# Performance work log

Hardware: AMD Instinct MI355X
Metric: run time of the kernel (lower is better)

The kernel has to match this reference:

```python
import jax, jax.numpy as jnp
import numpy as np

HID, NQ, NKV, HD = 4096, 32, 8, 128
EPS = 1e-6
GOLDEN = 1.618033988749895
BASE = 10000.0


def _rmsnorm(x, w, eps=EPS):
    var = jnp.mean(x.astype(jnp.float32) ** 2, axis=-1, keepdims=True)
    return (x * jax.lax.rsqrt(var + eps)).astype(x.dtype) * w


def _rope_half(t, pos, inv_freq):
    # t: (B,T,H,dh); pos: (B,T); inv_freq: (dh//2,)
    ang = pos.astype(jnp.float32)[..., None] * inv_freq  # (B,T,dq)
    cos = jnp.cos(ang)[:, :, None, :]
    sin = jnp.sin(ang)[:, :, None, :]
    dq = inv_freq.shape[0]
    t1, t2 = t[..., :dq], t[..., dq:]
    return jnp.concatenate([t1 * cos - t2 * sin, t1 * sin + t2 * cos], axis=-1)


def _apply_ggrope(q, k, row_ids, col_ids):
    # 2D RoPE: first half of head_dim encodes rows, second half encodes cols;
    # column frequencies scaled by the golden ratio (GGRoPE).
    dh = HD // 2
    inv_freq = 1.0 / (BASE ** (jnp.arange(0, dh, 2, dtype=jnp.float32) / dh))
    inv_freq_col = inv_freq * GOLDEN

    def rot(t):
        tr = _rope_half(t[..., :dh], row_ids, inv_freq)
        tc = _rope_half(t[..., dh:], col_ids, inv_freq_col)
        return jnp.concatenate([tr, tc], axis=-1)

    return rot(q), rot(k)


def setup_inputs() -> dict:
    key = jax.random.key(0)
    ks = jax.random.split(key, 9)
    B, T = 1, 2048
    s = 0.02
    return {
        "x": jax.random.normal(ks[0], (B, T, HID), jnp.float32),
        "row_ids": jax.random.randint(ks[1], (B, T), 0, 30),
        "col_ids": jax.random.randint(ks[2], (B, T), 0, 30),
        "attention_mask": jnp.zeros((B, 1, T, T), jnp.float32),
        "Wq": jax.random.normal(ks[3], (HID, NQ * HD), jnp.float32) * s,
        "Wk": jax.random.normal(ks[4], (HID, NKV * HD), jnp.float32) * s,
        "Wv": jax.random.normal(ks[5], (HID, NKV * HD), jnp.float32) * s,
        "Wo": jax.random.normal(ks[6], (NQ * HD, HID), jnp.float32) * s,
        "q_norm_w": jnp.ones((HD,), jnp.float32),
        "k_norm_w": jnp.ones((HD,), jnp.float32),
    }


def reference(x, row_ids, col_ids, attention_mask, Wq, Wk, Wv, Wo, q_norm_w, k_norm_w):
    B, T, _ = x.shape
    group = NQ // NKV
    q = (x @ Wq).reshape(B, T, NQ, HD)
    k = (x @ Wk).reshape(B, T, NKV, HD)
    v = (x @ Wv).reshape(B, T, NKV, HD)
    q = _rmsnorm(q, q_norm_w)
    k = _rmsnorm(k, k_norm_w)
    q, k = _apply_ggrope(q, k, row_ids, col_ids)
    # expand KV heads to match query heads (GQA)
    k = jnp.repeat(k, group, axis=2)  # (B,T,NQ,HD)
    v = jnp.repeat(v, group, axis=2)
    q = q.transpose(0, 2, 1, 3)  # (B,NQ,T,HD)
    k = k.transpose(0, 2, 1, 3)
    v = v.transpose(0, 2, 1, 3)
    ssmax_scale = (HD ** -0.5) * np.log(max(T, 2)).astype(np.float32)
    scores = jnp.einsum("bhqd,bhkd->bhqk", q, k) * ssmax_scale
    scores = scores + attention_mask
    attn = jax.nn.softmax(scores.astype(jnp.float32), axis=-1).astype(q.dtype)
    out = jnp.einsum("bhqk,bhkd->bhqd", attn, v)
    out = out.transpose(0, 2, 1, 3).reshape(B, T, NQ * HD)
    return out @ Wo
```

## Files before the change

kernel.cpp:

```cpp
#include <hip/hip_runtime.h>
#include <hip/hip_bf16.h>

typedef unsigned short u16;
typedef __attribute__((ext_vector_type(8))) short bf16x8;
typedef __attribute__((ext_vector_type(4))) float f32x4;

#define LOG2E_F 1.4426950408889634f
#define QSCALE (0.08838834764831845f * 7.625595228825695f * 1.4426950408889634f)

__device__ __forceinline__ u16 f2bf(float f) {
  unsigned x = __float_as_uint(f);
  unsigned r = (x + 0x7fffu + ((x >> 16) & 1u)) >> 16;
  return (u16)r;
}
__device__ __forceinline__ float bf2f(u16 u) {
  return __uint_as_float(((unsigned)u) << 16);
}
__device__ __forceinline__ float exp2a(float x) {
  float r;
  asm("v_exp_f32 %0, %1" : "=v"(r) : "v"(x));
  return r;
}
__device__ __forceinline__ unsigned cvtpk(float lo, float hi) {
  unsigned r;
  asm("v_cvt_pk_bf16_f32 %0, %1, %2" : "=v"(r) : "v"(lo), "v"(hi));
  return r;
}

__device__ __forceinline__ void gload_lds16(const void* g, void* l) {
  __builtin_amdgcn_global_load_lds(
      (__attribute__((address_space(1))) void*)(g),
      (__attribute__((address_space(3))) void*)(l), 16, 0, 0);
}

__device__ __forceinline__ f32x4 mfma16(bf16x8 a, bf16x8 b, f32x4 c) {
  return __builtin_amdgcn_mfma_f32_16x16x32_bf16(a, b, c, 0, 0, 0);
}

__global__ __launch_bounds__(256) void prep(const float4* __restrict__ x,
                                            ushort4* __restrict__ xb,
                                            const float4* __restrict__ mask,
                                            int* __restrict__ flag,
                                            const int* __restrict__ row_ids,
                                            const int* __restrict__ col_ids,
                                            float4* __restrict__ trig) {
  int bid = blockIdx.x;
  if (bid < 8192) {
    size_t i = (size_t)bid * 256 + threadIdx.x;
    float4 v = x[i];
    ushort4 o;
    o.x = f2bf(v.x); o.y = f2bf(v.y); o.z = f2bf(v.z); o.w = f2bf(v.w);
    xb[i] = o;
  } else if (bid < 12288) {
    size_t i = (size_t)(bid - 8192) * 256 + threadIdx.x;
    float4 v = mask[i];
    if (v.x != 0.f || v.y != 0.f || v.z != 0.f || v.w != 0.f) atomicOr(flag, 1);
  } else {
    int idx = (bid - 12288) * 256 + threadIdx.x;
    int tok = idx >> 5, i = idx & 31;
    float inv = exp2f(-(float)i * 0.41524101186092030f);
    float ar = (float)row_ids[tok] * inv;
    float ac = (float)col_ids[tok] * inv * 1.618033988749895f;
    float4 o;
    o.x = cosf(ar); o.y = sinf(ar); o.z = cosf(ac); o.w = sinf(ac);
    trig[idx] = o;
  }
}

__global__ __launch_bounds__(256) void tcvt_all(const float* __restrict__ Wq,
                                                const float* __restrict__ Wk,
                                                const float* __restrict__ Wv,
                                                const float* __restrict__ Wo,
                                                u16* __restrict__ wqkvt,
                                                u16* __restrict__ wot) {
  __shared__ float t[64][65];
  int bid = blockIdx.x;
  const float* src;
  u16* dst;
  int N;
  if (bid < 4096)      { src = Wq; dst = wqkvt;                         N = 4096; }
  else if (bid < 5120) { src = Wk; dst = wqkvt + (size_t)4096 * 4096;   N = 1024; bid -= 4096; }
  else if (bid < 6144) { src = Wv; dst = wqkvt + (size_t)5120 * 4096;   N = 1024; bid -= 5120; }
  else                 { src = Wo; dst = wot;                           N = 4096; bid -= 6144; }
  int kt = bid & 63, nt = bid >> 6;
  int k0 = kt * 64, n0 = nt * 64;
  int tid = threadIdx.x;
#pragma unroll
  for (int it = 0; it < 16; ++it) {
    int idx = it * 256 + tid;
    int row = idx >> 6, col = idx & 63;
    t[row][col] = src[(size_t)(k0 + row) * N + n0 + col];
  }
  __syncthreads();
#pragma unroll
  for (int it = 0; it < 8; ++it) {
    int idx = it * 256 + tid;
    int nrow = idx >> 5, kc = idx & 31;
    ushort2 o;
    o.x = f2bf(t[kc * 2][nrow]);
    o.y = f2bf(t[kc * 2 + 1][nrow]);
    *(ushort2*)&dst[(size_t)(n0 + nrow) * 4096 + k0 + kc * 2] = o;
  }
}

__global__ __launch_bounds__(256) void rope_kernel(u16* __restrict__ qk,
                                                   const float4* __restrict__ trig,
                                                   const float* __restrict__ qw,
                                                   const float* __restrict__ kw) {
  const int tok = blockIdx.x;
  const int tid = threadIdx.x;
  const int w = tid >> 6, lane = tid & 63;
  float4 t4 = trig[tok * 32 + (lane & 31)];
  float sgn = (lane < 32) ? -1.0f : 1.0f;

  for (int it = 0; it < 10; ++it) {
    int hh = w + it * 4;
    bool isQ = (hh < 32);
    int colbase = isQ ? hh * 128 : 4096 + (hh - 32) * 128;
    const float* nw = isQ ? qw : kw;
    float scale = isQ ? QSCALE : 1.0f;
    u16* p = qk + (size_t)tok * 5120 + colbase;
    float v1 = bf2f(p[lane]);
    float v2 = bf2f(p[64 + lane]);
    float w1 = nw[lane], w2 = nw[64 + lane];
    float ss = v1 * v1 + v2 * v2;
    ss += __shfl_xor(ss, 1);  ss += __shfl_xor(ss, 2);  ss += __shfl_xor(ss, 4);
    ss += __shfl_xor(ss, 8);  ss += __shfl_xor(ss, 16); ss += __shfl_xor(ss, 32);
    float rinv = rsqrtf(ss * (1.0f / 128.0f) + 1e-6f);
    float n1 = v1 * rinv * w1;
    float n2 = v2 * rinv * w2;
    float p1 = __shfl_xor(n1, 32);
    float p2 = __shfl_xor(n2, 32);
    float r1 = n1 * t4.x + sgn * p1 * t4.y;
    float r2 = n2 * t4.z + sgn * p2 * t4.w;
    p[lane]      = f2bf(r1 * scale);
    p[64 + lane] = f2bf(r2 * scale);
  }
}

template <int MODE>
__global__ __launch_bounds__(512, 2) void gemm256(const u16* __restrict__ A,
                                                  const u16* __restrict__ Bt,
                                                  void* __restrict__ C0,
                                                  u16* __restrict__ Vt, int nnt) {
  extern __shared__ char smem[];
  const int tid = threadIdx.x, lane = tid & 63, w = tid >> 6;
  const int l15 = lane & 15, l4 = lane >> 4;
  const int wr = w >> 2, wc = w & 3;
  constexpr int NF = (MODE == 0) ? 3 : 4;
  constexpr int BNW = (MODE == 0) ? 48 : 64;

  int wgid = (blockIdx.x & 7) * (gridDim.x >> 3) + (blockIdx.x >> 3);
  int kh = 0;
  if (MODE == 1) { kh = wgid >> 7; wgid &= 127; }
  const int mt = wgid / nnt, nt = wgid % nnt;
  const int m0 = mt * 256;
  const int n0 = nt * ((MODE == 0) ? 192 : 256);
  const int tbase = kh * 32;

  const int kswz = (((tid & 7) ^ ((tid >> 3) & 7)) << 4);
  const char* arow = (const char*)A + (size_t)(m0 + (tid >> 3)) * 8192 + kswz;
  const char* brow = (const char*)Bt + (size_t)(n0 + (tid >> 3)) * 8192 + kswz;

  auto stageA = [&](int t, int h) {
#pragma unroll
    for (int rd = 0; rd < 2; ++rd)
      gload_lds16(arow + (size_t)(h * 128 + rd * 64) * 8192 + t * 128,
                  smem + ((t & 1) * 2 + h) * 16384 + rd * 8192 + w * 1024);
  };
  auto stageB0 = [&](int t) {
#pragma unroll
    for (int rd = 0; rd < 3; ++rd)
      gload_lds16(brow + (size_t)(rd * 64) * 8192 + t * 128,
                  smem + 65536 + (t & 1) * 24576 + rd * 8192 + w * 1024);
  };
  auto stageB1 = [&](int t, int h) {
#pragma unroll
    for (int rd = 0; rd < 2; ++rd)
      gload_lds16(brow + (size_t)(h * 128 + rd * 64) * 8192 + t * 128,
                  smem + 65536 + ((t & 1) * 2 + h) * 16384 + rd * 8192 + w * 1024);
  };

  f32x4 acc[8][NF];
#pragma unroll
  for (int i = 0; i < 8; ++i)
#pragma unroll
    for (int j = 0; j < NF; ++j) acc[i][j] = (f32x4){0.f, 0.f, 0.f, 0.f};

  const int aoff0 = ((l4) ^ (l15 & 7)) << 4;
  const int aoff1 = ((4 + l4) ^ (l15 & 7)) << 4;

  stageA(tbase, 0); stageA(tbase, 1);
  if constexpr (MODE == 0) {
    stageB0(tbase); stageB0(tbase + 1);
    asm volatile("s_waitcnt vmcnt(3)" ::: "memory");
  } else {
    stageB1(tbase, 0); stageB1(tbase, 1);
    stageB1(tbase + 1, 0); stageB1(tbase + 1, 1);
    asm volatile("s_waitcnt vmcnt(4)" ::: "memory");
  }
  __builtin_amdgcn_s_barrier();

  auto do_iter = [&](int t0, int last) {
    bf16x8 bfr[NF][2];
#pragma unroll
    for (int p = 0; p < 8; ++p) {
      const int s = p >> 2, qd = p & 3;
      const char* aT = smem + (s * 2 + wr) * 16384 + l15 * 128;
      bf16x8 afr[2][2];
#pragma unroll
      for (int jm = 0; jm < 2; ++jm) {
        afr[jm][0] = *(const bf16x8*)(aT + (2 * qd + jm) * 2048 + aoff0);
        afr[jm][1] = *(const bf16x8*)(aT + (2 * qd + jm) * 2048 + aoff1);
      }
      if (qd == 0) {
        const char* bT;
        if constexpr (MODE == 0)
          bT = smem + 65536 + s * 24576 + (wc * 48 + l15) * 128;
        else
          bT = smem + 65536 + (s * 2 + (wc >> 1)) * 16384 +
               ((wc & 1) * 64 + l15) * 128;
#pragma unroll
        for (int nf = 0; nf < NF; ++nf) {
          bfr[nf][0] = *(const bf16x8*)(bT + nf * 2048 + aoff0);
          bfr[nf][1] = *(const bf16x8*)(bT + nf * 2048 + aoff1);
        }
      }
      if (p == 0) { stageA(t0 + 1, 0); stageA(t0 + 1, 1); }
      if (!last) {
        if constexpr (MODE == 0) {
          if (p == 1) stageB0(t0 + 2);
          if (p == 5) stageB0(t0 + 3);
        } else {
          if (p == 1) stageB1(t0 + 2, 0);
          if (p == 2) stageB1(t0 + 2, 1);
          if (p == 5) stageB1(t0 + 3, 0);
          if (p == 6) stageB1(t0 + 3, 1);
        }
        if (p == 4) { stageA(t0 + 2, 0); stageA(t0 + 2, 1); }
      }
      if (p == 3) {
        if (last) asm volatile("s_waitcnt vmcnt(0)" ::: "memory");
        else if constexpr (MODE == 0)
          asm volatile("s_waitcnt vmcnt(3)" ::: "memory");
        else
          asm volatile("s_waitcnt vmcnt(4)" ::: "memory");
      }
      if (p == 7 && !last) {
        if constexpr (MODE == 0)
          asm volatile("s_waitcnt vmcnt(3)" ::: "memory");
        else
          asm volatile("s_waitcnt vmcnt(4)" ::: "memory");
      }
      __builtin_amdgcn_s_barrier();
      asm volatile("s_waitcnt lgkmcnt(0)" ::: "memory");
      __builtin_amdgcn_sched_barrier(0);
      __builtin_amdgcn_s_setprio(1);
#pragma unroll
      for (int ks = 0; ks < 2; ++ks)
#pragma unroll
        for (int jm = 0; jm < 2; ++jm)
#pragma unroll
          for (int nf = 0; nf < NF; ++nf)
            acc[2 * qd + jm][nf] =
                mfma16(afr[jm][ks], bfr[nf][ks], acc[2 * qd + jm][nf]);
      __builtin_amdgcn_s_setprio(0);
      __builtin_amdgcn_s_barrier();
    }
  };

  constexpr int NIT = (MODE == 0) ? 32 : 16;
  for (int j = 0; j < NIT - 1; ++j) do_iter(tbase + 2 * j, 0);
  do_iter(tbase + 2 * (NIT - 1), 1);

  if (MODE == 0) {
    u16* qkp = (u16*)C0;
#pragma unroll
    for (int mf = 0; mf < 8; ++mf)
#pragma unroll
      for (int nf = 0; nf < NF; ++nf) {
        int ng = n0 + wc * BNW + nf * 16 + l15;
        if (ng < 5120) {
#pragma unroll
          for (int r = 0; r < 4; ++r) {
            int mg = m0 + wr * 128 + mf * 16 + l4 * 4 + r;
            qkp[(size_t)mg * 5120 + ng] = f2bf(acc[mf][nf][r]);
          }
        } else {
          int vr = ng - 5120;
          int mg = m0 + wr * 128 + mf * 16 + l4 * 4;
          ushort4 pk;
          pk.x = f2bf(acc[mf][nf][0]); pk.y = f2bf(acc[mf][nf][1]);
          pk.z = f2bf(acc[mf][nf][2]); pk.w = f2bf(acc[mf][nf][3]);
          *(ushort4*)&Vt[(size_t)vr * 2048 + mg] = pk;
        }
      }
  } else {
    float* Cp = (float*)C0 + (size_t)kh * 8388608;
#pragma unroll
    for (int mf = 0; mf < 8; ++mf)
#pragma unroll
      for (int nf = 0; nf < NF; ++nf) {
        int ng = n0 + wc * BNW + nf * 16 + l15;
#pragma unroll
        for (int r = 0; r < 4; ++r) {
          int mg = m0 + wr * 128 + mf * 16 + l4 * 4 + r;
          Cp[(size_t)mg * 4096 + ng] = acc[mf][nf][r];
        }
      }
  }
}

__global__ __launch_bounds__(256) void reduce2(const float4* __restrict__ p0,
                                               const float4* __restrict__ p1,
                                               float4* __restrict__ out) {
  size_t i = (size_t)blockIdx.x * 256 + threadIdx.x;
  float4 a = p0[i], b = p1[i];
  float4 o;
  o.x = a.x + b.x; o.y = a.y + b.y; o.z = a.z + b.z; o.w = a.w + b.w;
  out[i] = o;
}

__global__ __launch_bounds__(256, 2) void attn_kernel(const u16* __restrict__ qk,
                                                      const u16* __restrict__ vt,
                                                      u16* __restrict__ oat,
                                                      const float* __restrict__ mask,
                                                      const int* __restrict__ flag) {
  __shared__ u16 k_lds[2][64 * 128];
  __shared__ u16 v_lds[2][64 * 128];

  const int tid = threadIdx.x, lane = tid & 63, w = tid >> 6;
  const int l15 = lane & 15, l4 = lane >> 4;
  const int bid = blockIdx.x;
  const int hk = bid & 7;
  const int rest = bid >> 3;
  const int h = hk * 4 + (rest & 3);
  const int qt = rest >> 2;
  const int qbase = qt * 128 + w * 32;

  const bool use_mask = (*flag != 0);
  const char* kbase = (const char*)qk + 8192 + (size_t)hk * 256;
  const char* vbase = (const char*)vt + (size_t)hk * 128 * 4096;

  bf16x8 qf[2][4];
#pragma unroll
  for (int qg = 0; qg < 2; ++qg) {
    const char* qp = (const char*)qk +
                     (size_t)(qbase + qg * 16 + l15) * 10240 + h * 256 + l4 * 16;
#pragma unroll
    for (int ks = 0; ks < 4; ++ks) qf[qg][ks] = *(const bf16x8*)(qp + ks * 64);
  }

  f32x4 oacc[2][8];
#pragma unroll
  for (int qg = 0; qg < 2; ++qg)
#pragma unroll
    for (int fd = 0; fd < 8; ++fd) oacc[qg][fd] = (f32x4){0.f, 0.f, 0.f, 0.f};
  float m_run[2] = {-1e30f, -1e30f};
  float l_run[2] = {0.f, 0.f};

  int koff[4], voff[2];
#pragma unroll
  for (int ks = 0; ks < 4; ++ks) koff[ks] = ((4 * ks + l4) ^ l15) << 4;
#pragma unroll
  for (int ks = 0; ks < 2; ++ks) voff[ks] = ((4 * ks + l4) ^ (l15 & 7)) << 4;

#define STAGE(buf, kv0)                                                        \
  {                                                                            \
    _Pragma("unroll") for (int rd = 0; rd < 4; ++rd) {                         \
      int c = rd * 256 + tid;                                                  \
      int row = c >> 4;                                                        \
      int src = ((c & 15) ^ (row & 15)) << 4;                                  \
      gload_lds16(kbase + (size_t)((kv0) + row) * 10240 + src,                 \
                  (char*)k_lds[buf] + (rd * 256 + w * 64) * 16);               \
      int rowv = c >> 3;                                                       \
      int srcv = ((c & 7) ^ (rowv & 7)) << 4;                                  \
      gload_lds16(vbase + (size_t)rowv * 4096 + (kv0) * 2 + srcv,              \
                  (char*)v_lds[buf] + (rd * 256 + w * 64) * 16);               \
    }                                                                          \
  }

  STAGE(0, 0);
  asm volatile("s_waitcnt vmcnt(0)" ::: "memory");
  __builtin_amdgcn_s_barrier();
  __builtin_amdgcn_sched_barrier(0);

  for (int kt = 0; kt < 32; ++kt) {
    const int cur = kt & 1;
    const int kv0 = kt * 64;
    if (kt < 31) STAGE(cur ^ 1, kv0 + 64);

    f32x4 sA[2][4];
#pragma unroll
    for (int qg = 0; qg < 2; ++qg)
#pragma unroll
      for (int f = 0; f < 4; ++f) sA[qg][f] = (f32x4){0.f, 0.f, 0.f, 0.f};

    __builtin_amdgcn_s_setprio(1);
#pragma unroll
    for (int ks = 0; ks < 4; ++ks) {
      bf16x8 kfr[4];
#pragma unroll
      for (int f = 0; f < 4; ++f)
        kfr[f] = *(const bf16x8*)((const char*)k_lds[cur] +
                                  (16 * f + l15) * 256 + koff[ks]);
#pragma unroll
      for (int f = 0; f < 4; ++f) {
        sA[0][f] = mfma16(kfr[f], qf[0][ks], sA[0][f]);
        sA[1][f] = mfma16(kfr[f], qf[1][ks], sA[1][f]);
      }
    }
    __builtin_amdgcn_s_setprio(0);

    if (use_mask) {
#pragma unroll
      for (int qg = 0; qg < 2; ++qg) {
        int qglob = qbase + qg * 16 + l15;
#pragma unroll
        for (int f = 0; f < 4; ++f)
#pragma unroll
          for (int r = 0; r < 4; ++r) {
            int kvglob = kv0 + 16 * f + 4 * l4 + r;
            sA[qg][f][r] += LOG2E_F * mask[(size_t)qglob * 2048 + kvglob];
          }
      }
    }

    unsigned paw[2][2][4];
#pragma unroll
    for (int qg = 0; qg < 2; ++qg) {
      float mx = fmaxf(fmaxf(fmaxf(sA[qg][0][0], sA[qg][0][1]),
                             fmaxf(sA[qg][0][2], sA[qg][0][3])),
                       fmaxf(fmaxf(sA[qg][1][0], sA[qg][1][1]),
                             fmaxf(sA[qg][1][2], sA[qg][1][3])));
      float mx2 = fmaxf(fmaxf(fmaxf(sA[qg][2][0], sA[qg][2][1]),
                              fmaxf(sA[qg][2][2], sA[qg][2][3])),
                        fmaxf(fmaxf(sA[qg][3][0], sA[qg][3][1]),
                              fmaxf(sA[qg][3][2], sA[qg][3][3])));
      mx = fmaxf(mx, mx2);
      mx = fmaxf(mx, __shfl_xor(mx, 16));
      mx = fmaxf(mx, __shfl_xor(mx, 32));
      if (__any(mx > m_run[qg] + 8.0f)) {
        float mnew = fmaxf(m_run[qg], mx);
        float a = exp2a(m_run[qg] - mnew);
        l_run[qg] *= a;
        m_run[qg] = mnew;
        float a0 = __shfl(a, 4 * l4 + 0);
        float a1 = __shfl(a, 4 * l4 + 1);
        float a2 = __shfl(a, 4 * l4 + 2);
        float a3 = __shfl(a, 4 * l4 + 3);
#pragma unroll
        for (int fd = 0; fd < 8; ++fd) {
          oacc[qg][fd][0] *= a0; oacc[qg][fd][1] *= a1;
          oacc[qg][fd][2] *= a2; oacc[qg][fd][3] *= a3;
        }
      }
      float ps = 0.f;
      unsigned W[4][2];
#pragma unroll
      for (int f = 0; f < 4; ++f) {
        float p0 = exp2a(sA[qg][f][0] - m_run[qg]);
        float p1 = exp2a(sA[qg][f][1] - m_run[qg]);
        float p2 = exp2a(sA[qg][f][2] - m_run[qg]);
        float p3 = exp2a(sA[qg][f][3] - m_run[qg]);
        ps += (p0 + p1) + (p2 + p3);
        W[f][0] = cvtpk(p0, p1);
        W[f][1] = cvtpk(p2, p3);
      }
      ps += __shfl_xor(ps, 16);
      ps += __shfl_xor(ps, 32);
      l_run[qg] += ps;
#pragma unroll
      for (int ks = 0; ks < 2; ++ks)
#pragma unroll
        for (int wd = 0; wd < 4; ++wd) {
          int src = l15 + 16 * (2 * (l4 & 1) + (wd >> 1));
          unsigned v0 = (unsigned)__shfl((int)W[2 * ks][wd & 1], src);
          unsigned v1 = (unsigned)__shfl((int)W[2 * ks + 1][wd & 1], src);
          paw[qg][ks][wd] = (l4 & 2) ? v1 : v0;
        }
    }

    __builtin_amdgcn_s_setprio(1);
#pragma unroll
    for (int ks = 0; ks < 2; ++ks) {
      union { unsigned u[4]; bf16x8 v; } pa0, pa1;
#pragma unroll
      for (int wd = 0; wd < 4; ++wd) {
        pa0.u[wd] = paw[0][ks][wd];
        pa1.u[wd] = paw[1][ks][wd];
      }
#pragma unroll
      for (int fd = 0; fd < 8; ++fd) {
        bf16x8 vb = *(const bf16x8*)((const char*)v_lds[cur] +
                                     (16 * fd + l15) * 128 + voff[ks]);
        oacc[0][fd] = mfma16(pa0.v, vb, oacc[0][fd]);
        oacc[1][fd] = mfma16(pa1.v, vb, oacc[1][fd]);
      }
    }
    __builtin_amdgcn_s_setprio(0);

    if (kt < 31) {
      asm volatile("s_waitcnt vmcnt(0)" ::: "memory");
      __builtin_amdgcn_s_barrier();
      __builtin_amdgcn_sched_barrier(0);
    }
  }

#pragma unroll
  for (int qg = 0; qg < 2; ++qg) {
    float inv[4];
#pragma unroll
    for (int r = 0; r < 4; ++r) inv[r] = 1.0f / __shfl(l_run[qg], 4 * l4 + r);
#pragma unroll
    for (int fd = 0; fd < 8; ++fd) {
      int dg = h * 128 + 16 * fd + l15;
#pragma unroll
      for (int r = 0; r < 4; ++r) {
        int qrow = qbase + qg * 16 + 4 * l4 + r;
        oat[(size_t)qrow * 4096 + dg] = f2bf(oacc[qg][fd][r] * inv[r]);
      }
    }
  }
#undef STAGE
}

extern "C" void kernel_launch(void* const* d_in, const int* in_sizes, int n_in,
                              void* d_out, int out_size, void* d_ws, size_t ws_size,
                              hipStream_t stream) {
  const float* x = (const float*)d_in[0];
  const int* row_ids = (const int*)d_in[1];
  const int* col_ids = (const int*)d_in[2];
  const float* mask = (const float*)d_in[3];
  const float* Wq = (const float*)d_in[4];
  const float* Wk = (const float*)d_in[5];
  const float* Wv = (const float*)d_in[6];
  const float* Wo = (const float*)d_in[7];
  const float* qw = (const float*)d_in[8];
  const float* kw = (const float*)d_in[9];

  char* ws = (char*)d_ws;
  u16* xb      = (u16*)(ws);
  u16* wqkvt   = (u16*)(ws + 16777216);
  u16* wot     = (u16*)(ws + 67108864);
  u16* qkbuf   = (u16*)(ws + 100663296);
  u16* vtbuf   = (u16*)(ws + 121634816);
  u16* oat     = (u16*)(ws + 125829120);
  float4* trig = (float4*)(ws + 142606336);
  int* flag    = (int*)(ws + 143654912);
  float* pbuf  = (float*)(ws);

  hipFuncSetAttribute((const void*)gemm256<0>,
                      hipFuncAttributeMaxDynamicSharedMemorySize, 131072);
  hipFuncSetAttribute((const void*)gemm256<1>,
                      hipFuncAttributeMaxDynamicSharedMemorySize, 131072);

  hipMemsetAsync(flag, 0, 4, stream);
  prep<<<12544, 256, 0, stream>>>((const float4*)x, (ushort4*)xb,
                                  (const float4*)mask, flag, row_ids, col_ids,
                                  trig);
  tcvt_all<<<10240, 256, 0, stream>>>(Wq, Wk, Wv, Wo, wqkvt, wot);
  gemm256<0><<<256, 512, 114688, stream>>>(xb, wqkvt, (void*)qkbuf, vtbuf, 32);
  rope_kernel<<<2048, 256, 0, stream>>>(qkbuf, trig, qw, kw);
  attn_kernel<<<512, 256, 0, stream>>>(qkbuf, vtbuf, oat, mask, flag);
  gemm256<1><<<256, 512, 131072, stream>>>(oat, wot, (void*)pbuf, nullptr, 16);
  reduce2<<<8192, 256, 0, stream>>>((const float4*)pbuf,
                                    (const float4*)(pbuf + 8388608),
                                    (float4*)d_out);
}
```

Measured before the change: 346.2 us.

## Single-buffer attention LDS, raise occupancy, and use 16x16x16 MFMA for PV

The attention kernel drops K/V LDS double buffering in favour of a single buffer and raises launch bounds from 2 to 4 blocks per CU. The P·V product now uses v_mfma_f32_16x16x16_bf16 fed directly from the softmax register layout, which removes the cross-lane shuffle that repacked P into the 16x16x32 operand layout. In exchange, the K/V load for the next tile is no longer overlapped with compute inside a block, so the design relies on more resident blocks to hide memory latency. The narrower MFMA also needs twice as many PV instructions.

```diff
diff --git a/kernel.cpp b/kernel.cpp
--- a/kernel.cpp
+++ b/kernel.cpp
@@ -3,6 +3,7 @@
 
 typedef unsigned short u16;
 typedef __attribute__((ext_vector_type(8))) short bf16x8;
+typedef __attribute__((ext_vector_type(4))) short bf16x4;
 typedef __attribute__((ext_vector_type(4))) float f32x4;
 
 #define LOG2E_F 1.4426950408889634f
@@ -35,6 +36,9 @@
 
 __device__ __forceinline__ f32x4 mfma16(bf16x8 a, bf16x8 b, f32x4 c) {
   return __builtin_amdgcn_mfma_f32_16x16x32_bf16(a, b, c, 0, 0, 0);
+}
+__device__ __forceinline__ void mfma16x16(f32x4& c, bf16x4 a, bf16x4 b) {
+  asm("v_mfma_f32_16x16x16_bf16 %0, %1, %2, %0" : "+v"(c) : "v"(a), "v"(b));
 }
 
 __global__ __launch_bounds__(256) void prep(const float4* __restrict__ x,
@@ -321,13 +325,13 @@
   out[i] = o;
 }
 
-__global__ __launch_bounds__(256, 2) void attn_kernel(const u16* __restrict__ qk,
+__global__ __launch_bounds__(256, 4) void attn_kernel(const u16* __restrict__ qk,
                                                       const u16* __restrict__ vt,
                                                       u16* __restrict__ oat,
                                                       const float* __restrict__ mask,
                                                       const int* __restrict__ flag) {
-  __shared__ u16 k_lds[2][64 * 128];
-  __shared__ u16 v_lds[2][64 * 128];
+  __shared__ u16 k_lds[64 * 128];
+  __shared__ u16 v_lds[64 * 128];
 
   const int tid = threadIdx.x, lane = tid & 63, w = tid >> 6;
   const int l15 = lane & 15, l4 = lane >> 4;
@@ -359,36 +363,35 @@
   float m_run[2] = {-1e30f, -1e30f};
   float l_run[2] = {0.f, 0.f};
 
-  int koff[4], voff[2];
+  int koff[4], voff64[4];
 #pragma unroll
   for (int ks = 0; ks < 4; ++ks) koff[ks] = ((4 * ks + l4) ^ l15) << 4;
 #pragma unroll
-  for (int ks = 0; ks < 2; ++ks) voff[ks] = ((4 * ks + l4) ^ (l15 & 7)) << 4;
-
-#define STAGE(buf, kv0)                                                        \
+  for (int f = 0; f < 4; ++f)
+    voff64[f] = (((2 * f + (l4 >> 1)) ^ (l15 & 7)) << 4) + 8 * (l4 & 1);
+
+#define STAGE(kv0)                                                             \
   {                                                                            \
     _Pragma("unroll") for (int rd = 0; rd < 4; ++rd) {                         \
       int c = rd * 256 + tid;                                                  \
       int row = c >> 4;                                                        \
       int src = ((c & 15) ^ (row & 15)) << 4;                                  \
       gload_lds16(kbase + (size_t)((kv0) + row) * 10240 + src,                 \
-                  (char*)k_lds[buf] + (rd * 256 + w * 64) * 16);               \
+                  (char*)k_lds + (rd * 256 + w * 64) * 16);                    \
       int rowv = c >> 3;                                                       \
       int srcv = ((c & 7) ^ (rowv & 7)) << 4;                                  \
       gload_lds16(vbase + (size_t)rowv * 4096 + (kv0) * 2 + srcv,              \
-                  (char*)v_lds[buf] + (rd * 256 + w * 64) * 16);               \
+                  (char*)v_lds + (rd * 256 + w * 64) * 16);                    \
     }                                                                          \
   }
 
-  STAGE(0, 0);
+  STAGE(0);
   asm volatile("s_waitcnt vmcnt(0)" ::: "memory");
   __builtin_amdgcn_s_barrier();
   __builtin_amdgcn_sched_barrier(0);
 
   for (int kt = 0; kt < 32; ++kt) {
-    const int cur = kt & 1;
     const int kv0 = kt * 64;
-    if (kt < 31) STAGE(cur ^ 1, kv0 + 64);
 
     f32x4 sA[2][4];
 #pragma unroll
@@ -402,7 +405,7 @@
       bf16x8 kfr[4];
 #pragma unroll
       for (int f = 0; f < 4; ++f)
-        kfr[f] = *(const bf16x8*)((const char*)k_lds[cur] +
+        kfr[f] = *(const bf16x8*)((const char*)k_lds +
                                   (16 * f + l15) * 256 + koff[ks]);
 #pragma unroll
       for (int f = 0; f < 4; ++f) {
@@ -426,7 +429,7 @@
       }
     }
 
-    unsigned paw[2][2][4];
+    unsigned W[2][4][2];
 #pragma unroll
     for (int qg = 0; qg < 2; ++qg) {
       float mx = fmaxf(fmaxf(fmaxf(sA[qg][0][0], sA[qg][0][1]),
@@ -456,7 +459,6 @@
         }
       }
       float ps = 0.f;
-      unsigned W[4][2];
 #pragma unroll
       for (int f = 0; f < 4; ++f) {
         float p0 = exp2a(sA[qg][f][0] - m_run[qg]);
@@ -464,43 +466,34 @@
         float p2 = exp2a(sA[qg][f][2] - m_run[qg]);
         float p3 = exp2a(sA[qg][f][3] - m_run[qg]);
         ps += (p0 + p1) + (p2 + p3);
-        W[f][0] = cvtpk(p0, p1);
-        W[f][1] = cvtpk(p2, p3);
+        W[qg][f][0] = cvtpk(p0, p1);
+        W[qg][f][1] = cvtpk(p2, p3);
       }
       ps += __shfl_xor(ps, 16);
       ps += __shfl_xor(ps, 32);
       l_run[qg] += ps;
-#pragma unroll
-      for (int ks = 0; ks < 2; ++ks)
-#pragma unroll
-        for (int wd = 0; wd < 4; ++wd) {
-          int src = l15 + 16 * (2 * (l4 & 1) + (wd >> 1));
-          unsigned v0 = (unsigned)__shfl((int)W[2 * ks][wd & 1], src);
-          unsigned v1 = (unsigned)__shfl((int)W[2 * ks + 1][wd & 1], src);
-          paw[qg][ks][wd] = (l4 & 2) ? v1 : v0;
-        }
     }
 
     __builtin_amdgcn_s_setprio(1);
 #pragma unroll
-    for (int ks = 0; ks < 2; ++ks) {
-      union { unsigned u[4]; bf16x8 v; } pa0, pa1;
-#pragma unroll
-      for (int wd = 0; wd < 4; ++wd) {
-        pa0.u[wd] = paw[0][ks][wd];
-        pa1.u[wd] = paw[1][ks][wd];
-      }
+    for (int f = 0; f < 4; ++f) {
+      union { unsigned u[2]; bf16x4 v; } pa0, pa1;
+      pa0.u[0] = W[0][f][0]; pa0.u[1] = W[0][f][1];
+      pa1.u[0] = W[1][f][0]; pa1.u[1] = W[1][f][1];
 #pragma unroll
       for (int fd = 0; fd < 8; ++fd) {
-        bf16x8 vb = *(const bf16x8*)((const char*)v_lds[cur] +
-                                     (16 * fd + l15) * 128 + voff[ks]);
-        oacc[0][fd] = mfma16(pa0.v, vb, oacc[0][fd]);
-        oacc[1][fd] = mfma16(pa1.v, vb, oacc[1][fd]);
+        bf16x4 vb = *(const bf16x4*)((const char*)v_lds +
+                                     (16 * fd + l15) * 128 + voff64[f]);
+        mfma16x16(oacc[0][fd], pa0.v, vb);
+        mfma16x16(oacc[1][fd], pa1.v, vb);
       }
     }
     __builtin_amdgcn_s_setprio(0);
 
+    asm volatile("s_waitcnt lgkmcnt(0)" ::: "memory");
+    __builtin_amdgcn_s_barrier();
     if (kt < 31) {
+      STAGE(kv0 + 64);
       asm volatile("s_waitcnt vmcnt(0)" ::: "memory");
       __builtin_amdgcn_s_barrier();
       __builtin_amdgcn_sched_barrier(0);
```

New measurement: 528.5 us. 52.7% more time.

## Split attention over KV halves with flash-decoding style combine kernel

Applied to the files above, without the earlier changes.

Attention now launches twice as many blocks, each covering half of the KV sequence, and writes unnormalized fp32 partial outputs plus per-row max and sum to workspace. A new combine kernel merges the two halves and emits the bf16 attention output. LDS double buffering is replaced by a single buffer with an extra barrier per tile, which is meant to cut LDS use so more blocks fit per CU. The cost is extra global traffic for the fp32 partials, an additional launch, and loss of load/compute overlap inside each block.

```diff
diff --git a/kernel.cpp b/kernel.cpp
--- a/kernel.cpp
+++ b/kernel.cpp
@@ -323,20 +323,23 @@
 
 __global__ __launch_bounds__(256, 2) void attn_kernel(const u16* __restrict__ qk,
                                                       const u16* __restrict__ vt,
-                                                      u16* __restrict__ oat,
+                                                      float* __restrict__ opart,
+                                                      float2* __restrict__ ml,
                                                       const float* __restrict__ mask,
                                                       const int* __restrict__ flag) {
-  __shared__ u16 k_lds[2][64 * 128];
-  __shared__ u16 v_lds[2][64 * 128];
+  __shared__ u16 k_lds[64 * 128];
+  __shared__ u16 v_lds[64 * 128];
 
   const int tid = threadIdx.x, lane = tid & 63, w = tid >> 6;
   const int l15 = lane & 15, l4 = lane >> 4;
   const int bid = blockIdx.x;
   const int hk = bid & 7;
-  const int rest = bid >> 3;
+  const int ks2 = (bid >> 3) & 1;
+  const int rest = bid >> 4;
   const int h = hk * 4 + (rest & 3);
   const int qt = rest >> 2;
   const int qbase = qt * 128 + w * 32;
+  const int kvbase = ks2 * 1024;
 
   const bool use_mask = (*flag != 0);
   const char* kbase = (const char*)qk + 8192 + (size_t)hk * 256;
@@ -365,30 +368,28 @@
 #pragma unroll
   for (int ks = 0; ks < 2; ++ks) voff[ks] = ((4 * ks + l4) ^ (l15 & 7)) << 4;
 
-#define STAGE(buf, kv0)                                                        \
+#define STAGE(kv0)                                                             \
   {                                                                            \
     _Pragma("unroll") for (int rd = 0; rd < 4; ++rd) {                         \
       int c = rd * 256 + tid;                                                  \
       int row = c >> 4;                                                        \
       int src = ((c & 15) ^ (row & 15)) << 4;                                  \
       gload_lds16(kbase + (size_t)((kv0) + row) * 10240 + src,                 \
-                  (char*)k_lds[buf] + (rd * 256 + w * 64) * 16);               \
+                  (char*)k_lds + (rd * 256 + w * 64) * 16);                    \
       int rowv = c >> 3;                                                       \
       int srcv = ((c & 7) ^ (rowv & 7)) << 4;                                  \
       gload_lds16(vbase + (size_t)rowv * 4096 + (kv0) * 2 + srcv,              \
-                  (char*)v_lds[buf] + (rd * 256 + w * 64) * 16);               \
+                  (char*)v_lds + (rd * 256 + w * 64) * 16);                    \
     }                                                                          \
   }
 
-  STAGE(0, 0);
+  STAGE(kvbase);
   asm volatile("s_waitcnt vmcnt(0)" ::: "memory");
   __builtin_amdgcn_s_barrier();
   __builtin_amdgcn_sched_barrier(0);
 
-  for (int kt = 0; kt < 32; ++kt) {
-    const int cur = kt & 1;
-    const int kv0 = kt * 64;
-    if (kt < 31) STAGE(cur ^ 1, kv0 + 64);
+  for (int kt = 0; kt < 16; ++kt) {
+    const int kv0 = kvbase + kt * 64;
 
     f32x4 sA[2][4];
 #pragma unroll
@@ -402,7 +403,7 @@
       bf16x8 kfr[4];
 #pragma unroll
       for (int f = 0; f < 4; ++f)
-        kfr[f] = *(const bf16x8*)((const char*)k_lds[cur] +
+        kfr[f] = *(const bf16x8*)((const char*)k_lds +
                                   (16 * f + l15) * 256 + koff[ks]);
 #pragma unroll
       for (int f = 0; f < 4; ++f) {
@@ -492,7 +493,7 @@
       }
 #pragma unroll
       for (int fd = 0; fd < 8; ++fd) {
-        bf16x8 vb = *(const bf16x8*)((const char*)v_lds[cur] +
+        bf16x8 vb = *(const bf16x8*)((const char*)v_lds +
                                      (16 * fd + l15) * 128 + voff[ks]);
         oacc[0][fd] = mfma16(pa0.v, vb, oacc[0][fd]);
         oacc[1][fd] = mfma16(pa1.v, vb, oacc[1][fd]);
@@ -500,29 +501,56 @@
     }
     __builtin_amdgcn_s_setprio(0);
 
-    if (kt < 31) {
+    asm volatile("s_waitcnt lgkmcnt(0)" ::: "memory");
+    __builtin_amdgcn_s_barrier();
+    if (kt < 15) {
+      STAGE(kv0 + 64);
       asm volatile("s_waitcnt vmcnt(0)" ::: "memory");
       __builtin_amdgcn_s_barrier();
       __builtin_amdgcn_sched_barrier(0);
     }
   }
 
+  float* op = opart + (size_t)ks2 * 8388608;
 #pragma unroll
   for (int qg = 0; qg < 2; ++qg) {
-    float inv[4];
-#pragma unroll
-    for (int r = 0; r < 4; ++r) inv[r] = 1.0f / __shfl(l_run[qg], 4 * l4 + r);
 #pragma unroll
     for (int fd = 0; fd < 8; ++fd) {
       int dg = h * 128 + 16 * fd + l15;
 #pragma unroll
       for (int r = 0; r < 4; ++r) {
         int qrow = qbase + qg * 16 + 4 * l4 + r;
-        oat[(size_t)qrow * 4096 + dg] = f2bf(oacc[qg][fd][r] * inv[r]);
-      }
+        op[(size_t)qrow * 4096 + dg] = oacc[qg][fd][r];
+      }
+    }
+    if (l4 == 0) {
+      int qrow = qbase + qg * 16 + l15;
+      ml[((size_t)ks2 * 32 + h) * 2048 + qrow] = make_float2(m_run[qg], l_run[qg]);
     }
   }
 #undef STAGE
+}
+
+__global__ __launch_bounds__(256) void combine(const float4* __restrict__ o0,
+                                               const float4* __restrict__ o1,
+                                               const float2* __restrict__ ml,
+                                               ushort4* __restrict__ oat) {
+  size_t i = (size_t)blockIdx.x * 256 + threadIdx.x;
+  int q = (int)(i >> 10);
+  int h = ((int)i & 1023) >> 5;
+  float2 ml0 = ml[(size_t)h * 2048 + q];
+  float2 ml1 = ml[((size_t)32 + h) * 2048 + q];
+  float mm = fmaxf(ml0.x, ml1.x);
+  float a0 = exp2a(ml0.x - mm), a1 = exp2a(ml1.x - mm);
+  float inv = 1.0f / (a0 * ml0.y + a1 * ml1.y);
+  float s0 = a0 * inv, s1 = a1 * inv;
+  float4 v0 = o0[i], v1 = o1[i];
+  ushort4 o;
+  o.x = f2bf(v0.x * s0 + v1.x * s1);
+  o.y = f2bf(v0.y * s0 + v1.y * s1);
+  o.z = f2bf(v0.z * s0 + v1.z * s1);
+  o.w = f2bf(v0.w * s0 + v1.w * s1);
+  oat[i] = o;
 }
 
 extern "C" void kernel_launch(void* const* d_in, const int* in_sizes, int n_in,
@@ -548,6 +576,8 @@
   u16* oat     = (u16*)(ws + 125829120);
   float4* trig = (float4*)(ws + 142606336);
   int* flag    = (int*)(ws + 143654912);
+  float* opart = (float*)(ws);
+  float2* ml   = (float2*)(ws + 142606336);
   float* pbuf  = (float*)(ws);
 
   hipFuncSetAttribute((const void*)gemm256<0>,
@@ -562,7 +592,10 @@
   tcvt_all<<<10240, 256, 0, stream>>>(Wq, Wk, Wv, Wo, wqkvt, wot);
   gemm256<0><<<256, 512, 114688, stream>>>(xb, wqkvt, (void*)qkbuf, vtbuf, 32);
   rope_kernel<<<2048, 256, 0, stream>>>(qkbuf, trig, qw, kw);
-  attn_kernel<<<512, 256, 0, stream>>>(qkbuf, vtbuf, oat, mask, flag);
+  attn_kernel<<<1024, 256, 0, stream>>>(qkbuf, vtbuf, opart, ml, mask, flag);
+  combine<<<8192, 256, 0, stream>>>((const float4*)opart,
+                                    (const float4*)(opart + 8388608), ml,
+                                    (ushort4*)oat);
   gemm256<1><<<256, 512, 131072, stream>>>(oat, wot, (void*)pbuf, nullptr, 16);
   reduce2<<<8192, 256, 0, stream>>>((const float4*)pbuf,
                                     (const float4*)(pbuf + 8388608),
```

Result: slower. 366.4 us (+5.8%).
